# Kernel optimization log

Measured on AMD Instinct MI355X. Metric: run time of the kernel, lower is better.

Reference implementation:

```python
import jax, jax.numpy as jnp
import numpy as np
import math

N = 50000   # nodes
E = 800000  # edges
D = 128     # in_channels == out_channels
SLOPE = 0.1
BN_EPS = 1e-5


def setup_inputs() -> dict:
    key = jax.random.key(0)
    k1, k2, k3 = jax.random.split(key, 3)
    x = jax.random.normal(k1, (N, D), jnp.float32)
    edge_index = jax.random.randint(k2, (2, E), 0, N, jnp.int32)
    # xavier_uniform with leaky_relu gain, as in reset_parameters
    gain = math.sqrt(2.0 / (1.0 + SLOPE ** 2))
    bound = gain * math.sqrt(6.0 / (D + D))
    W = jax.random.uniform(k3, (D, D), jnp.float32, -bound, bound)  # lin.weight [out,in]
    bias = jnp.zeros((D,), jnp.float32)
    gamma = jnp.ones((D,), jnp.float32)
    beta = jnp.zeros((D,), jnp.float32)
    return {"x": x, "W": W, "bias": bias, "gamma": gamma, "beta": beta,
            "edge_index": edge_index}


def reference(x, W, bias, gamma, beta, edge_index):
    n = x.shape[0]
    residual = x  # shortcut is Identity (in_channels == out_channels)

    loops = jnp.arange(n, dtype=edge_index.dtype)
    self_loops = jnp.stack([loops, loops])

    # forward() manually adds self-loops and computes symmetric norm (edge_weight)
    ei1 = jnp.concatenate([edge_index, self_loops], axis=1)
    row1, col1 = ei1[0], ei1[1]
    deg = jax.ops.segment_sum(jnp.ones_like(row1, x.dtype), row1, n)
    dis = jnp.where(deg > 0, jax.lax.rsqrt(jnp.where(deg > 0, deg, 1.0)), 0.0)
    w1 = dis[row1] * dis[col1]

    # GCNConv(normalize=True, improved=True) internally re-runs gcn_norm:
    # adds another set of self-loops with fill_value 2.0, recomputes sym norm
    ei2 = jnp.concatenate([ei1, self_loops], axis=1)
    w2 = jnp.concatenate([w1, jnp.full((n,), 2.0, x.dtype)])
    row2, col2 = ei2[0], ei2[1]
    deg2 = jax.ops.segment_sum(w2, col2, n)
    dis2 = jnp.where(deg2 > 0, jax.lax.rsqrt(jnp.where(deg2 > 0, deg2, 1.0)), 0.0)
    norm = dis2[row2] * w2 * dis2[col2]

    # linear transform then gather-scale-scatter aggregation
    h = x @ W.T                                           # [N, D]
    agg = jax.ops.segment_sum(norm[:, None] * h[row2], col2, n) + bias

    # BatchNorm1d (training-mode batch stats), LeakyReLU, dropout (eval=identity)
    mu = agg.mean(axis=0)
    var = agg.var(axis=0)
    bn = (agg - mu) * jax.lax.rsqrt(var + BN_EPS) * gamma + beta
    act = jax.nn.leaky_relu(bn, SLOPE)
    return jax.nn.leaky_relu(act + residual, SLOPE)
```

## Files before the change

### kernel.cpp

```cpp
#include <hip/hip_runtime.h>
#include <hip/hip_fp16.h>

constexpr float SLOPE = 0.1f;
constexpr float BN_EPS = 1e-5f;
constexpr int BCAP = 8192;
constexpr int CHUNK = 4096;
constexpr int BKT = 1024;
constexpr int EPT = CHUNK / BKT;

typedef __attribute__((ext_vector_type(8))) short bf16x8;
typedef __attribute__((ext_vector_type(4))) float f32x4;
typedef __attribute__((ext_vector_type(2))) float f32x2;

__device__ inline unsigned bf16rn(float f) {
    unsigned b = __float_as_uint(f);
    return (b + 0x7fffu + ((b >> 16) & 1u)) >> 16;
}

__device__ inline unsigned h2u(__half2 h) { return *(unsigned*)&h; }
__device__ inline __half2 u2h(unsigned u) { return *(__half2*)&u; }

__global__ void k_zero(int* __restrict__ p, int n) {
    int i = blockIdx.x * blockDim.x + threadIdx.x;
    if (i < n) p[i] = 0;
}

__global__ __launch_bounds__(1024) void k_bucket3(const int* __restrict__ row,
                                                  const int* __restrict__ col, int E,
                                                  int* __restrict__ bcnt, int* __restrict__ rcnt,
                                                  unsigned* __restrict__ bdat,
                                                  unsigned char* __restrict__ rdat, int NB) {
    __shared__ unsigned sdata[CHUNK];
    __shared__ int cnt[256];
    __shared__ int off[256];
    __shared__ int gbase[256];
    __shared__ int wsum[4];
    int t = threadIdx.x;
    int l = t & 63, w = t >> 6;
    int base = blockIdx.x * CHUNK;
    int total = min(E - base, CHUNK);
    int r[EPT], c[EPT];
#pragma unroll
    for (int k = 0; k < EPT; ++k) {
        int i = base + k * BKT + t;
        if (i < E) { r[k] = row[i]; c[k] = col[i]; } else { r[k] = -1; c[k] = 0; }
    }
    if (t < 256) cnt[t] = 0;
    __syncthreads();
#pragma unroll
    for (int k = 0; k < EPT; ++k) if (r[k] >= 0) atomicAdd(&cnt[c[k] >> 8], 1);
    __syncthreads();
    int v = (t < 256) ? cnt[t] : 0, inc = v;
#pragma unroll
    for (int d = 1; d < 64; d <<= 1) { int u = __shfl_up(inc, d); if (l >= d) inc += u; }
    if (t < 256 && l == 63) wsum[w] = inc;
    __syncthreads();
    if (t < 256) {
        int p = 0;
        for (int i = 0; i < w; ++i) p += wsum[i];
        off[t] = p + inc - v;
        cnt[t] = 0;
    }
    __syncthreads();
#pragma unroll
    for (int k = 0; k < EPT; ++k) if (r[k] >= 0) {
        int bb = c[k] >> 8;
        int pos = off[bb] + atomicAdd(&cnt[bb], 1);
        sdata[pos] = ((unsigned)r[k] << 8) | (unsigned)(c[k] & 255);
    }
    __syncthreads();
    if (t < NB) gbase[t] = atomicAdd(&bcnt[t * 16], cnt[t]);
    __syncthreads();
    for (int i = t; i < total; i += BKT) {
        int b = 0;
#pragma unroll
        for (int stp = 128; stp > 0; stp >>= 1) {
            int cand = b + stp;
            if (cand < 256 && off[cand] <= i) b = cand;
        }
        int pos = gbase[b] + (i - off[b]);
        if (pos < BCAP) bdat[(size_t)b * BCAP + pos] = sdata[i];
    }
    __syncthreads();
    unsigned char* sb = (unsigned char*)sdata;
    if (t < 256) cnt[t] = 0;
    __syncthreads();
#pragma unroll
    for (int k = 0; k < EPT; ++k) if (r[k] >= 0) atomicAdd(&cnt[r[k] >> 8], 1);
    __syncthreads();
    v = (t < 256) ? cnt[t] : 0; inc = v;
#pragma unroll
    for (int d = 1; d < 64; d <<= 1) { int u = __shfl_up(inc, d); if (l >= d) inc += u; }
    if (t < 256 && l == 63) wsum[w] = inc;
    __syncthreads();
    if (t < 256) {
        int p = 0;
        for (int i = 0; i < w; ++i) p += wsum[i];
        off[t] = p + inc - v;
        cnt[t] = 0;
    }
    __syncthreads();
#pragma unroll
    for (int k = 0; k < EPT; ++k) if (r[k] >= 0) {
        int rb = r[k] >> 8;
        int pos = off[rb] + atomicAdd(&cnt[rb], 1);
        sb[pos] = (unsigned char)(r[k] & 255);
    }
    __syncthreads();
    if (t < NB) gbase[t] = atomicAdd(&rcnt[t * 16], cnt[t]);
    __syncthreads();
    for (int i = t; i < total; i += BKT) {
        int b = 0;
#pragma unroll
        for (int stp = 128; stp > 0; stp >>= 1) {
            int cand = b + stp;
            if (cand < 256 && off[cand] <= i) b = cand;
        }
        int pos = gbase[b] + (i - off[b]);
        if (pos < BCAP) rdat[(size_t)b * BCAP + pos] = sb[i];
    }
}

__global__ __launch_bounds__(512) void k_outdeg(const int* __restrict__ rcnt,
                                                const unsigned char* __restrict__ rdat,
                                                float* __restrict__ dis, int N) {
    __shared__ int hist[256];
    int b = blockIdx.x, t = threadIdx.x;
    if (t < 256) hist[t] = 0;
    __syncthreads();
    int cnt = min(rcnt[b * 16], BCAP);
    const unsigned char* p = rdat + (size_t)b * BCAP;
    const unsigned* p4 = (const unsigned*)p;
    int nw = cnt >> 2;
    for (int i = t; i < nw; i += 512) {
        unsigned v = p4[i];
        atomicAdd(&hist[v & 255u], 1);
        atomicAdd(&hist[(v >> 8) & 255u], 1);
        atomicAdd(&hist[(v >> 16) & 255u], 1);
        atomicAdd(&hist[v >> 24], 1);
    }
    for (int i = nw * 4 + t; i < cnt; i += 512) atomicAdd(&hist[p[i]], 1);
    __syncthreads();
    if (t < 256) {
        int node = b * 256 + t;
        if (node < N) dis[node] = rsqrtf((float)(hist[t] + 1));
    }
}

__global__ __launch_bounds__(512) void k_deg2(const int* __restrict__ bcnt,
                                              const unsigned* __restrict__ bdat,
                                              const float* __restrict__ dis,
                                              int* __restrict__ csr_off,
                                              float* __restrict__ dw,
                                              float* __restrict__ selfw, int N, int NB) {
    __shared__ int   hist[256];
    __shared__ float fsum[256];
    __shared__ int   sm2[256];
    __shared__ int   sm2x[256];
    __shared__ int   wsum[4];
    int b = blockIdx.x, t = threadIdx.x;
    int l = t & 63, w = t >> 6;
    if (t < 256) {
        sm2[t] = (t < NB) ? min(bcnt[t * 16], BCAP) : 0;
        hist[t] = 0;
        fsum[t] = 0.0f;
    }
    __syncthreads();
    int v = (t < 256) ? sm2[t] : 0, inc = v;
#pragma unroll
    for (int d = 1; d < 64; d <<= 1) { int u = __shfl_up(inc, d); if (l >= d) inc += u; }
    if (t < 256 && l == 63) wsum[w] = inc;
    __syncthreads();
    if (t < 256) {
        int p = 0;
        for (int i = 0; i < w; ++i) p += wsum[i];
        sm2x[t] = p + inc - v;
    }
    __syncthreads();
    if (b == 0 && t == 0) csr_off[N] = sm2x[NB - 1] + sm2[NB - 1];
    int bb = sm2x[b];
    int cnt = min(bcnt[b * 16], BCAP);
    const unsigned* p = bdat + (size_t)b * BCAP;
    for (int i = t; i < cnt; i += 512) {
        unsigned e = p[i];
        int c = (int)(e & 255u);
        atomicAdd(&hist[c], 1);
        atomicAdd(&fsum[c], dis[e >> 8]);
    }
    __syncthreads();
    v = (t < 256) ? hist[t] : 0; inc = v;
#pragma unroll
    for (int d = 1; d < 64; d <<= 1) { int u = __shfl_up(inc, d); if (l >= d) inc += u; }
    if (t < 256 && l == 63) wsum[w] = inc;
    __syncthreads();
    if (t < 256) {
        int p2 = 0;
        for (int i = 0; i < w; ++i) p2 += wsum[i];
        int node = b * 256 + t;
        if (node < N) {
            csr_off[node] = bb + p2 + inc - v;
            float ds = dis[node];
            float deg2 = 2.0f + ds * ds + ds * fsum[t];
            dw[node] = ds * rsqrtf(deg2);
            selfw[node] = (ds * ds + 2.0f) / deg2;
        }
    }
}

__global__ __launch_bounds__(512) void k_csr2(const int* __restrict__ bcnt,
                                              const unsigned* __restrict__ bdat,
                                              const int* __restrict__ csr_off,
                                              const float* __restrict__ dw,
                                              unsigned* __restrict__ csr, int N, int NB) {
    __shared__ int   tick[256];
    __shared__ int   base[256];
    __shared__ float dwl[256];
    int b = blockIdx.x, t = threadIdx.x;
    if (t < 256) {
        tick[t] = 0;
        int node = b * 256 + t;
        base[t] = (node < N) ? csr_off[node] : 0;
        dwl[t]  = (node < N) ? dw[node] : 0.0f;
    }
    __syncthreads();
    int cnt = min(bcnt[b * 16], BCAP);
    const unsigned* p = bdat + (size_t)b * BCAP;
    for (int i = t; i < cnt; i += 512) {
        unsigned e = p[i];
        int c = (int)(e & 255u);
        int r = (int)(e >> 8);
        float wgt = dw[r] * dwl[c];
        int pos = base[c] + atomicAdd(&tick[c], 1);
        unsigned hb = (unsigned)__half_as_ushort(__float2half_rn(wgt));
        csr[pos] = ((unsigned)r << 16) | hb;
    }
}

__global__ __launch_bounds__(256) void k_gemm(const float* __restrict__ x,
                                              const float* __restrict__ W,
                                              unsigned* __restrict__ h16,
                                              unsigned* __restrict__ h8, int N) {
    __shared__ unsigned short wb[128 * 136];
    int tx = threadIdx.x;
    for (int idx = tx; idx < 128 * 64; idx += 256) {
        int d = idx >> 6;
        int kp = (idx & 63) * 2;
        float2 wv = *(const float2*)&W[d * 128 + kp];
        wb[d * 136 + kp]     = (unsigned short)bf16rn(wv.x);
        wb[d * 136 + kp + 1] = (unsigned short)bf16rn(wv.y);
    }
    __syncthreads();
    int wave = tx >> 6, l = tx & 63;
    int lr = l & 15, kg = l >> 4;
    int row = blockIdx.x * 64 + wave * 16 + lr;
    int rclamp = min(row, N - 1);
    f32x4 acc[8];
#pragma unroll
    for (int ct = 0; ct < 8; ++ct) acc[ct] = (f32x4){0.f, 0.f, 0.f, 0.f};
#pragma unroll
    for (int kt = 0; kt < 4; ++kt) {
        int k0 = kt * 32 + kg * 8;
        float xv[8];
        *(float4*)&xv[0] = *(const float4*)&x[(size_t)rclamp * 128 + k0];
        *(float4*)&xv[4] = *(const float4*)&x[(size_t)rclamp * 128 + k0 + 4];
        bf16x8 a;
#pragma unroll
        for (int j = 0; j < 8; ++j) a[j] = (short)bf16rn(xv[j]);
#pragma unroll
        for (int ct = 0; ct < 8; ++ct) {
            bf16x8 bfr = *(const bf16x8*)&wb[(ct * 16 + lr) * 136 + k0];
            acc[ct] = __builtin_amdgcn_mfma_f32_16x16x32_bf16(a, bfr, acc[ct], 0, 0, 0);
        }
    }
    int rowbase = blockIdx.x * 64 + wave * 16 + kg * 4;
#pragma unroll
    for (int ct = 0; ct < 8; ++ct) {
#pragma unroll
        for (int reg = 0; reg < 4; ++reg) {
            float v = acc[ct][reg];
            float p1 = __shfl_xor(v, 1);
            float p2 = __shfl_xor(v, 2);
            float p3 = __shfl_xor(v, 3);
            int orow = rowbase + reg;
            if (orow < N) {
                if ((l & 1) == 0) {
                    unsigned a0 = (unsigned)__half_as_ushort(__float2half_rn(v));
                    unsigned a1 = (unsigned)__half_as_ushort(__float2half_rn(p1));
                    h16[(size_t)orow * 64 + ct * 8 + (lr >> 1)] = a0 | (a1 << 16);
                }
                if ((l & 3) == 0) {
                    int wpk = 0;
                    wpk = __builtin_amdgcn_cvt_pk_fp8_f32(v, p1, wpk, false);
                    wpk = __builtin_amdgcn_cvt_pk_fp8_f32(p2, p3, wpk, true);
                    h8[(size_t)orow * 32 + ct * 4 + (lr >> 2)] = (unsigned)wpk;
                }
            }
        }
    }
}

__global__ __launch_bounds__(256) void k_agg(const uint2* __restrict__ h8,
                                             const uint4* __restrict__ h16,
                                             const int* __restrict__ csr_off,
                                             const unsigned* __restrict__ csr,
                                             const float* __restrict__ selfw,
                                             uint4* __restrict__ agg16, int N) {
    int wv = threadIdx.x >> 6;
    int l = threadIdx.x & 63;
    int ep = l >> 4;
    int sl = l & 15;
    int j = blockIdx.x * 4 + wv;
    if (j >= N) return;
    float acc[8] = {};
    int s0 = csr_off[j], s1 = csr_off[j + 1];
    for (int s = s0 + ep; s < s1; s += 16) {
        int sB = s + 4, sC = s + 8, sD = s + 12;
        unsigned eA = csr[s];
        unsigned eB = (sB < s1) ? csr[sB] : eA;
        unsigned eC = (sC < s1) ? csr[sC] : eA;
        unsigned eD = (sD < s1) ? csr[sD] : eA;
        float wA = __half2float(__ushort_as_half((unsigned short)(eA & 0xffffu)));
        float wB = (sB < s1) ? __half2float(__ushort_as_half((unsigned short)(eB & 0xffffu))) : 0.0f;
        float wC = (sC < s1) ? __half2float(__ushort_as_half((unsigned short)(eC & 0xffffu))) : 0.0f;
        float wD = (sD < s1) ? __half2float(__ushort_as_half((unsigned short)(eD & 0xffffu))) : 0.0f;
        uint2 aA = h8[(size_t)(eA >> 16) * 16 + sl];
        uint2 aB = h8[(size_t)(eB >> 16) * 16 + sl];
        uint2 aC = h8[(size_t)(eC >> 16) * 16 + sl];
        uint2 aD = h8[(size_t)(eD >> 16) * 16 + sl];
#define PACC(aa, ww) { \
        f32x2 q0 = __builtin_amdgcn_cvt_pk_f32_fp8((int)aa.x, false); \
        f32x2 q1 = __builtin_amdgcn_cvt_pk_f32_fp8((int)aa.x, true);  \
        f32x2 q2 = __builtin_amdgcn_cvt_pk_f32_fp8((int)aa.y, false); \
        f32x2 q3 = __builtin_amdgcn_cvt_pk_f32_fp8((int)aa.y, true);  \
        acc[0] += ww * q0.x; acc[1] += ww * q0.y; \
        acc[2] += ww * q1.x; acc[3] += ww * q1.y; \
        acc[4] += ww * q2.x; acc[5] += ww * q2.y; \
        acc[6] += ww * q3.x; acc[7] += ww * q3.y; }
        PACC(aA, wA)
        PACC(aB, wB)
        PACC(aC, wC)
        PACC(aD, wD)
#undef PACC
    }
#pragma unroll
    for (int k = 0; k < 8; ++k) {
        acc[k] += __shfl_xor(acc[k], 16);
        acc[k] += __shfl_xor(acc[k], 32);
    }
    if (ep == 0) {
        float sw = selfw[j];
        uint4 hv = h16[(size_t)j * 16 + sl];
        const __half2* hp = (const __half2*)&hv;
#pragma unroll
        for (int k = 0; k < 4; ++k) {
            float2 f = __half22float2(hp[k]);
            acc[2 * k]     += sw * f.x;
            acc[2 * k + 1] += sw * f.y;
        }
        uint4 o;
        o.x = h2u(__floats2half2_rn(acc[0], acc[1]));
        o.y = h2u(__floats2half2_rn(acc[2], acc[3]));
        o.z = h2u(__floats2half2_rn(acc[4], acc[5]));
        o.w = h2u(__floats2half2_rn(acc[6], acc[7]));
        agg16[(size_t)j * 16 + sl] = o;
    }
}

__global__ __launch_bounds__(1024) void k_stats(const __half2* __restrict__ agg2,
                                                float* __restrict__ sums, int N) {
    __shared__ float ls[256];
    int t = threadIdx.x;
    if (t < 256) ls[t] = 0.0f;
    __syncthreads();
    int d = t & 63;
    int stream = blockIdx.x * 16 + (t >> 6);
    int nstreams = gridDim.x * 16;
    float s0 = 0.f, s1 = 0.f, q0 = 0.f, q1 = 0.f;
    for (int i = stream; i < N; i += nstreams) {
        float2 f = __half22float2(agg2[(size_t)i * 64 + d]);
        s0 += f.x; s1 += f.y;
        q0 += f.x * f.x; q1 += f.y * f.y;
    }
    atomicAdd(&ls[2 * d], s0);
    atomicAdd(&ls[2 * d + 1], s1);
    atomicAdd(&ls[128 + 2 * d], q0);
    atomicAdd(&ls[128 + 2 * d + 1], q1);
    __syncthreads();
    if (t < 256) atomicAdd(&sums[t], ls[t]);
}

__global__ void k_final(const uint2* __restrict__ agg16, const float* __restrict__ x,
                        const float* __restrict__ sums, const float* __restrict__ gamma,
                        const float* __restrict__ beta, float* __restrict__ out,
                        int total4, int N) {
    __shared__ float sc[128], sh[128];
    int t = threadIdx.x;
    if (t < 128) {
        float invN = 1.0f / (float)N;
        float mu = sums[t] * invN;
        float var = sums[128 + t] * invN - mu * mu;
        float s = gamma[t] * rsqrtf(var + BN_EPS);
        sc[t] = s;
        sh[t] = beta[t] - mu * s;
    }
    __syncthreads();
    int idx = blockIdx.x * blockDim.x + t;
    if (idx >= total4) return;
    int c4 = (idx & 31) * 4;
    uint2 a2 = agg16[idx];
    float2 f0 = __half22float2(u2h(a2.x));
    float2 f1 = __half22float2(u2h(a2.y));
    float4 xv = *(const float4*)&x[(size_t)idx * 4];
    float ap[4] = {f0.x, f0.y, f1.x, f1.y};
    float xp[4] = {xv.x, xv.y, xv.z, xv.w};
    float op[4];
#pragma unroll
    for (int j = 0; j < 4; ++j) {
        int d = c4 + j;
        float bn = ap[j] * sc[d] + sh[d];
        float act = bn > 0.0f ? bn : SLOPE * bn;
        float v = act + xp[j];
        op[j] = v > 0.0f ? v : SLOPE * v;
    }
    *(float4*)&out[(size_t)idx * 4] = make_float4(op[0], op[1], op[2], op[3]);
}

extern "C" void kernel_launch(void* const* d_in, const int* in_sizes, int n_in,
                              void* d_out, int out_size, void* d_ws, size_t ws_size,
                              hipStream_t stream) {
    const float* x     = (const float*)d_in[0];
    const float* W     = (const float*)d_in[1];
    const float* gamma = (const float*)d_in[3];
    const float* beta  = (const float*)d_in[4];
    const int*   ei    = (const int*)d_in[5];
    int N = in_sizes[0] / 128;
    int E = in_sizes[5] / 2;
    const int* row = ei;
    const int* col = ei + E;
    float* out = (float*)d_out;

    int NB = (N + 255) >> 8;

    char* ws = (char*)d_ws;
    size_t off = 0;
    auto alloc = [&](size_t b) { size_t o = off; off = (off + b + 255) & ~(size_t)255; return o; };
    size_t o_sums  = alloc(512 * 4);
    size_t o_bcnt  = alloc((size_t)NB * 16 * 4);
    size_t o_rcnt  = alloc((size_t)NB * 16 * 4);
    size_t zbytes  = off;
    size_t o_bdat  = alloc((size_t)NB * BCAP * 4);
    size_t o_rdat  = alloc((size_t)NB * BCAP);
    size_t o_dis   = alloc((size_t)N * 4);
    size_t o_dw    = alloc((size_t)N * 4);
    size_t o_selfw = alloc((size_t)N * 4);
    size_t o_coff  = alloc((size_t)(N + 1) * 4);
    size_t o_crow  = alloc((size_t)E * 4);
    size_t o_h16   = alloc((size_t)N * 128 * 2);
    size_t o_h8    = alloc((size_t)N * 128);
    size_t o_agg   = alloc((size_t)N * 128 * 2);
    if (ws_size < off) return;

    float*         sums    = (float*)(ws + o_sums);
    int*           bcnt    = (int*)(ws + o_bcnt);
    int*           rcnt    = (int*)(ws + o_rcnt);
    unsigned*      bdat    = (unsigned*)(ws + o_bdat);
    unsigned char* rdat    = (unsigned char*)(ws + o_rdat);
    float*         dis     = (float*)(ws + o_dis);
    float*         dw      = (float*)(ws + o_dw);
    float*         selfw   = (float*)(ws + o_selfw);
    int*           csr_off = (int*)(ws + o_coff);
    unsigned*      csr     = (unsigned*)(ws + o_crow);
    unsigned*      h16     = (unsigned*)(ws + o_h16);
    unsigned*      h8      = (unsigned*)(ws + o_h8);
    unsigned*      agg     = (unsigned*)(ws + o_agg);

    int NBLK = (E + CHUNK - 1) / CHUNK;
    int zn = (int)(zbytes / 4);

    k_zero<<<(zn + 255) / 256, 256, 0, stream>>>((int*)ws, zn);
    k_bucket3<<<NBLK, BKT, 0, stream>>>(row, col, E, bcnt, rcnt, bdat, rdat, NB);
    k_outdeg<<<NB, 512, 0, stream>>>(rcnt, rdat, dis, N);
    k_deg2<<<NB, 512, 0, stream>>>(bcnt, bdat, dis, csr_off, dw, selfw, N, NB);
    k_csr2<<<NB, 512, 0, stream>>>(bcnt, bdat, csr_off, dw, csr, N, NB);
    k_gemm<<<(N + 63) / 64, 256, 0, stream>>>(x, W, h16, h8, N);
    k_agg<<<(N + 3) / 4, 256, 0, stream>>>((const uint2*)h8, (const uint4*)h16, csr_off, csr, selfw, (uint4*)agg, N);
    k_stats<<<128, 1024, 0, stream>>>((const __half2*)agg, sums, N);
    int total4 = N * 32;
    k_final<<<(total4 + 255) / 256, 256, 0, stream>>>((const uint2*)agg, x, sums, gamma, beta, out, total4, N);
}
```

Measured before the change: 112.8 us.

## Split fp8 feature table into two column halves and aggregate each half separately

The GEMM now writes the fp8 copy of h as two planes of 64 columns each, one after the other. The aggregation kernel launches twice as many waves, and each wave handles one column half of one node. Each half-row gather is 64 bytes read by 8 lanes, and the number of edges in flight per wave is unchanged. The aim is a smaller per-pass working set for the random gathers, so each half table is more likely to stay in cache. The cost is that every CSR row (offsets and edge entries) is now read twice.

```diff
diff --git a/kernel.cpp b/kernel.cpp
--- a/kernel.cpp
+++ b/kernel.cpp
@@ -292,7 +292,8 @@
                     int wpk = 0;
                     wpk = __builtin_amdgcn_cvt_pk_fp8_f32(v, p1, wpk, false);
                     wpk = __builtin_amdgcn_cvt_pk_fp8_f32(p2, p3, wpk, true);
-                    h8[(size_t)orow * 32 + ct * 4 + (lr >> 2)] = (unsigned)wpk;
+                    int wd = ct * 4 + (lr >> 2);
+                    h8[((size_t)(wd >> 4) * N + orow) * 16 + (wd & 15)] = (unsigned)wpk;
                 }
             }
         }
@@ -307,26 +308,23 @@
                                              uint4* __restrict__ agg16, int N) {
     int wv = threadIdx.x >> 6;
     int l = threadIdx.x & 63;
-    int ep = l >> 4;
-    int sl = l & 15;
-    int j = blockIdx.x * 4 + wv;
+    int ep = l >> 3;
+    int sl = l & 7;
+    int g = blockIdx.x * 4 + wv;
+    int half = (g >= N) ? 1 : 0;
+    int j = g - half * N;
     if (j >= N) return;
+    size_t hoff = (size_t)half * N;
     float acc[8] = {};
     int s0 = csr_off[j], s1 = csr_off[j + 1];
     for (int s = s0 + ep; s < s1; s += 16) {
-        int sB = s + 4, sC = s + 8, sD = s + 12;
+        int s2 = s + 8;
         unsigned eA = csr[s];
-        unsigned eB = (sB < s1) ? csr[sB] : eA;
-        unsigned eC = (sC < s1) ? csr[sC] : eA;
-        unsigned eD = (sD < s1) ? csr[sD] : eA;
+        unsigned eB = (s2 < s1) ? csr[s2] : eA;
         float wA = __half2float(__ushort_as_half((unsigned short)(eA & 0xffffu)));
-        float wB = (sB < s1) ? __half2float(__ushort_as_half((unsigned short)(eB & 0xffffu))) : 0.0f;
-        float wC = (sC < s1) ? __half2float(__ushort_as_half((unsigned short)(eC & 0xffffu))) : 0.0f;
-        float wD = (sD < s1) ? __half2float(__ushort_as_half((unsigned short)(eD & 0xffffu))) : 0.0f;
-        uint2 aA = h8[(size_t)(eA >> 16) * 16 + sl];
-        uint2 aB = h8[(size_t)(eB >> 16) * 16 + sl];
-        uint2 aC = h8[(size_t)(eC >> 16) * 16 + sl];
-        uint2 aD = h8[(size_t)(eD >> 16) * 16 + sl];
+        float wB = (s2 < s1) ? __half2float(__ushort_as_half((unsigned short)(eB & 0xffffu))) : 0.0f;
+        uint2 aA = h8[(hoff + (eA >> 16)) * 8 + sl];
+        uint2 aB = h8[(hoff + (eB >> 16)) * 8 + sl];
 #define PACC(aa, ww) { \
         f32x2 q0 = __builtin_amdgcn_cvt_pk_f32_fp8((int)aa.x, false); \
         f32x2 q1 = __builtin_amdgcn_cvt_pk_f32_fp8((int)aa.x, true);  \
@@ -338,18 +336,17 @@
         acc[6] += ww * q3.x; acc[7] += ww * q3.y; }
         PACC(aA, wA)
         PACC(aB, wB)
-        PACC(aC, wC)
-        PACC(aD, wD)
 #undef PACC
     }
 #pragma unroll
     for (int k = 0; k < 8; ++k) {
+        acc[k] += __shfl_xor(acc[k], 8);
         acc[k] += __shfl_xor(acc[k], 16);
         acc[k] += __shfl_xor(acc[k], 32);
     }
     if (ep == 0) {
         float sw = selfw[j];
-        uint4 hv = h16[(size_t)j * 16 + sl];
+        uint4 hv = h16[(size_t)j * 16 + half * 8 + sl];
         const __half2* hp = (const __half2*)&hv;
 #pragma unroll
         for (int k = 0; k < 4; ++k) {
@@ -362,7 +359,7 @@
         o.y = h2u(__floats2half2_rn(acc[2], acc[3]));
         o.z = h2u(__floats2half2_rn(acc[4], acc[5]));
         o.w = h2u(__floats2half2_rn(acc[6], acc[7]));
-        agg16[(size_t)j * 16 + sl] = o;
+        agg16[(size_t)j * 16 + half * 8 + sl] = o;
     }
 }
 
@@ -483,7 +480,8 @@
     k_deg2<<<NB, 512, 0, stream>>>(bcnt, bdat, dis, csr_off, dw, selfw, N, NB);
     k_csr2<<<NB, 512, 0, stream>>>(bcnt, bdat, csr_off, dw, csr, N, NB);
     k_gemm<<<(N + 63) / 64, 256, 0, stream>>>(x, W, h16, h8, N);
-    k_agg<<<(N + 3) / 4, 256, 0, stream>>>((const uint2*)h8, (const uint4*)h16, csr_off, csr, selfw, (uint4*)agg, N);
+    int ngg = (2 * N + 3) / 4;
+    k_agg<<<ngg, 256, 0, stream>>>((const uint2*)h8, (const uint4*)h16, csr_off, csr, selfw, (uint4*)agg, N);
     k_stats<<<128, 1024, 0, stream>>>((const __half2*)agg, sums, N);
     int total4 = N * 32;
     k_final<<<(total4 + 255) / 256, 256, 0, stream>>>((const uint2*)agg, x, sums, gamma, beta, out, total4, N);
```

After: 129.0 us. +14.4%, slower.
